# Optimization experiments

Measured on AMD Instinct MI355X. Metric: run time of the kernel, lower is better.

Reference implementation:

```python
import jax, jax.numpy as jnp
import numpy as np

N = 8192      # number of tokens/nodes
D = 256       # out_dim
E = N - 1     # one dependency triple per non-root node
ALPHA = 0.2   # LeakyReLU negative slope


def setup_inputs() -> dict:
    key = jax.random.key(0)
    k1, k2, k3, k4 = jax.random.split(key, 4)
    x = jax.random.normal(k1, (N, D), jnp.float32)
    W = jax.random.normal(k2, (D, D), jnp.float32) / np.sqrt(D)      # nn.Linear(out,out,bias=False).weight
    a = jax.random.normal(k3, (2 * D,), jnp.float32) / np.sqrt(2 * D)  # nn.Linear(2*out,1,bias=False).weight
    # each node 1..N-1 is a dependent exactly once -> h_dict keys are [0,1,...,N-1] in order
    dep = jnp.arange(1, N, dtype=jnp.int32)
    # each governor appears at most once -> each e_tensor row is softmaxed exactly once
    gov = jax.random.permutation(k4, N)[:E].astype(jnp.int32)
    return {"x": x, "W": W, "a": a, "dep": dep, "gov": gov}


def reference(x, W, a, dep, gov):
    Nn, Dd = x.shape
    neg_big = jnp.asarray(-1e18, x.dtype)
    Hx = x @ W.T  # self.weight(x[i]) for every node, [N, D]
    # per-edge attention logit: attn_weight(cat(W x_gov, W x_dep))
    s = jnp.concatenate([Hx[gov], Hx[dep]], axis=-1) @ a  # [E]
    # dense e_tensor exactly as in the module
    e = jnp.zeros((Nn, Nn), x.dtype).at[gov, dep].set(s)
    # rows belonging to a governor get masked softmax; other rows untouched
    gov_mask = jnp.zeros((Nn,), bool).at[gov].set(True)
    masked = jnp.where(e > 0, e, neg_big)
    sm = jax.nn.softmax(masked, axis=1)
    attn = jnp.where(gov_mask[:, None], sm, e)
    # self_loop/h_dict init: h[dep] = W x[gov]; node 0 stays zeros
    h = jnp.zeros((Nn, Dd), x.dtype).at[dep].set(Hx[gov])
    # aggregation: h[gov] += attn[gov, dep] * W x[dep]
    coef = attn[gov, dep]  # [E]
    h = h + jax.ops.segment_sum(coef[:, None] * Hx[dep], gov, num_segments=Nn)
    return jax.nn.leaky_relu(h, ALPHA)
```

## Files before the change

### kernel.cpp

```cpp
#include <hip/hip_runtime.h>
#include <hip/hip_bf16.h>

#define NN 8192
#define DD 256
#define EE (NN - 1)

typedef __attribute__((ext_vector_type(8))) short bf16x8;
typedef __attribute__((ext_vector_type(4))) float f32x4;

__device__ inline unsigned short f2bf(float f) {
  return __builtin_bit_cast(unsigned short, __float2bfloat16(f));
}

__global__ __launch_bounds__(1024) void prep(
    const float* __restrict__ W, const float* __restrict__ a,
    const int* __restrict__ gov,
    float* __restrict__ u, float* __restrict__ v, int* __restrict__ inv) {
  const int t = threadIdx.x;
  const int k = t & 255, part = t >> 8;

  for (int i = t; i < NN; i += 1024) inv[i] = -1;
  __syncthreads();
  for (int e = t; e < EE; e += 1024) inv[gov[e]] = e;

  float up = 0.f, vp = 0.f;
  const int j0 = part * 64;
  for (int j = j0; j < j0 + 64; ++j) {
    float w = W[(size_t)j * DD + k];
    up = fmaf(a[j], w, up);
    vp = fmaf(a[DD + j], w, vp);
  }
  __shared__ float redu[4][256], redv[4][256];
  redu[part][k] = up; redv[part][k] = vp;
  __syncthreads();
  if (t < 256) {
    u[t] = redu[0][t] + redu[1][t] + redu[2][t] + redu[3][t];
    v[t] = redv[0][t] + redv[1][t] + redv[2][t] + redv[3][t];
  }
}

__global__ __launch_bounds__(256) void pq_kernel(
    const float* __restrict__ x, const float* __restrict__ u,
    const float* __restrict__ v, float* __restrict__ p, float* __restrict__ q) {
  const int wid = threadIdx.x >> 6, lane = threadIdx.x & 63;
  const int row = blockIdx.x * 4 + wid;
  const float4 xv = *(const float4*)&x[(size_t)row * DD + lane * 4];
  const float4 uv = *(const float4*)&u[lane * 4];
  const float4 vv = *(const float4*)&v[lane * 4];
  float ps = xv.x * uv.x + xv.y * uv.y + xv.z * uv.z + xv.w * uv.w;
  float qs = xv.x * vv.x + xv.y * vv.y + xv.z * vv.z + xv.w * vv.w;
#pragma unroll
  for (int off = 32; off; off >>= 1) {
    ps += __shfl_xor(ps, off);
    qs += __shfl_xor(qs, off);
  }
  if (lane == 0) { p[row] = ps; q[row] = qs; }
}

#define BM 128
#define BN 64
#define BK 32
#define LDAB 40

__global__ __launch_bounds__(256) void gemm_mfma(
    const float* __restrict__ X, const float* __restrict__ W,
    float* __restrict__ Hx) {
  __shared__ unsigned short As[BM][LDAB];
  __shared__ unsigned short Bs[BN][LDAB];
  const int t = threadIdx.x;
  const int bm = blockIdx.x * BM, bn = blockIdx.y * BN;
  const int lane = t & 63;
  const int wid = t >> 6;
  const int wr = wid >> 1, wc = wid & 1;
  const int l15 = lane & 15, l4 = lane >> 4;

  f32x4 acc[4][2] = {};

  const int arow = t >> 1, ahalf = t & 1;
  const int brow = t >> 2, bq = t & 3;

  for (int k0 = 0; k0 < DD; k0 += BK) {
    {
      const float* src = &X[(size_t)(bm + arow) * DD + k0 + ahalf * 16];
#pragma unroll
      for (int i = 0; i < 4; ++i) {
        float4 f = *(const float4*)(src + i * 4);
        ushort4 pk;
        pk.x = f2bf(f.x); pk.y = f2bf(f.y); pk.z = f2bf(f.z); pk.w = f2bf(f.w);
        *(ushort4*)&As[arow][ahalf * 16 + i * 4] = pk;
      }
    }
    {
      const float* src = &W[(size_t)(bn + brow) * DD + k0 + bq * 8];
#pragma unroll
      for (int i = 0; i < 2; ++i) {
        float4 f = *(const float4*)(src + i * 4);
        ushort4 pk;
        pk.x = f2bf(f.x); pk.y = f2bf(f.y); pk.z = f2bf(f.z); pk.w = f2bf(f.w);
        *(ushort4*)&Bs[brow][bq * 8 + i * 4] = pk;
      }
    }
    __syncthreads();

    bf16x8 af[4], bfr[2];
#pragma unroll
    for (int mf = 0; mf < 4; ++mf)
      af[mf] = *(const bf16x8*)&As[wr * 64 + mf * 16 + l15][l4 * 8];
#pragma unroll
    for (int nf = 0; nf < 2; ++nf)
      bfr[nf] = *(const bf16x8*)&Bs[wc * 32 + nf * 16 + l15][l4 * 8];
#pragma unroll
    for (int mf = 0; mf < 4; ++mf)
#pragma unroll
      for (int nf = 0; nf < 2; ++nf)
        acc[mf][nf] = __builtin_amdgcn_mfma_f32_16x16x32_bf16(
            af[mf], bfr[nf], acc[mf][nf], 0, 0, 0);
    __syncthreads();
  }

#pragma unroll
  for (int mf = 0; mf < 4; ++mf)
#pragma unroll
    for (int nf = 0; nf < 2; ++nf)
#pragma unroll
      for (int r = 0; r < 4; ++r) {
        const int row = bm + wr * 64 + mf * 16 + l4 * 4 + r;
        const int col = bn + wc * 32 + nf * 16 + l15;
        Hx[(size_t)row * DD + col] = acc[mf][nf][r];
      }
}

__global__ __launch_bounds__(256) void finalize(
    const float* __restrict__ Hx, const float* __restrict__ p,
    const float* __restrict__ q, const int* __restrict__ gov,
    const int* __restrict__ inv, float* __restrict__ out) {
  const int sub = threadIdx.x >> 6, c4 = threadIdx.x & 63;
  const int j = blockIdx.x * 4 + sub;

  float4 h = make_float4(0.f, 0.f, 0.f, 0.f);
  if (j > 0) {
    const int g = gov[j - 1];
    h = *(const float4*)&Hx[(size_t)g * DD + c4 * 4];
  }
  const int e2 = inv[j];
  if (e2 >= 0) {
    const int d = e2 + 1;
    const float4 hd = *(const float4*)&Hx[(size_t)d * DD + c4 * 4];
    const float s = p[j] + q[d];
    const float coef = (s > 0.f) ? 1.f : (1.f / 8192.f);
    h.x = fmaf(coef, hd.x, h.x);
    h.y = fmaf(coef, hd.y, h.y);
    h.z = fmaf(coef, hd.z, h.z);
    h.w = fmaf(coef, hd.w, h.w);
  }
  float4 o;
  o.x = (h.x >= 0.f) ? h.x : 0.2f * h.x;
  o.y = (h.y >= 0.f) ? h.y : 0.2f * h.y;
  o.z = (h.z >= 0.f) ? h.z : 0.2f * h.z;
  o.w = (h.w >= 0.f) ? h.w : 0.2f * h.w;
  *(float4*)&out[(size_t)j * DD + c4 * 4] = o;
}

extern "C" void kernel_launch(void* const* d_in, const int* in_sizes, int n_in,
                              void* d_out, int out_size, void* d_ws, size_t ws_size,
                              hipStream_t stream) {
  const float* x = (const float*)d_in[0];
  const float* W = (const float*)d_in[1];
  const float* a = (const float*)d_in[2];
  const int* gov = (const int*)d_in[4];

  float* Hx = (float*)d_ws;
  float* p  = Hx + (size_t)NN * DD;
  float* q  = p + NN;
  float* u  = q + NN;
  float* v  = u + DD;
  int* inv  = (int*)(v + DD);

  hipLaunchKernelGGL(prep, dim3(1), dim3(1024), 0, stream, W, a, gov, u, v, inv);
  hipLaunchKernelGGL(pq_kernel, dim3(NN / 4), dim3(256), 0, stream, x, u, v, p, q);
  hipLaunchKernelGGL(gemm_mfma, dim3(NN / BM, DD / BN), dim3(256), 0, stream,
                     x, W, Hx);
  hipLaunchKernelGGL(finalize, dim3(NN / 4), dim3(256), 0, stream,
                     Hx, p, q, gov, inv, (float*)d_out);
}
```

Measured before the change: 101.4 us.

## Aggregate x rows before the projection GEMM and fuse LeakyReLU into its epilogue

```diff
diff --git a/kernel.cpp b/kernel.cpp
--- a/kernel.cpp
+++ b/kernel.cpp
@@ -25,6 +25,7 @@
 
   float up = 0.f, vp = 0.f;
   const int j0 = part * 64;
+#pragma unroll 4
   for (int j = j0; j < j0 + 64; ++j) {
     float w = W[(size_t)j * DD + k];
     up = fmaf(a[j], w, up);
@@ -57,60 +58,81 @@
   if (lane == 0) { p[row] = ps; q[row] = qs; }
 }
 
-#define BM 128
+__global__ __launch_bounds__(256) void combine(
+    const float* __restrict__ x, const float* __restrict__ p,
+    const float* __restrict__ q, const int* __restrict__ gov,
+    const int* __restrict__ inv, unsigned short* __restrict__ y) {
+  const int sub = threadIdx.x >> 6, lane = threadIdx.x & 63;
+  const int j = blockIdx.x * 4 + sub;
+
+  float4 h = make_float4(0.f, 0.f, 0.f, 0.f);
+  if (j > 0) {
+    const int g = gov[j - 1];
+    h = *(const float4*)&x[(size_t)g * DD + lane * 4];
+  }
+  const int e2 = inv[j];
+  if (e2 >= 0) {
+    const int d = e2 + 1;
+    const float4 xd = *(const float4*)&x[(size_t)d * DD + lane * 4];
+    const float s = p[j] + q[d];
+    const float coef = (s > 0.f) ? 1.f : (1.f / 8192.f);
+    h.x = fmaf(coef, xd.x, h.x);
+    h.y = fmaf(coef, xd.y, h.y);
+    h.z = fmaf(coef, xd.z, h.z);
+    h.w = fmaf(coef, xd.w, h.w);
+  }
+  ushort4 pk;
+  pk.x = f2bf(h.x); pk.y = f2bf(h.y); pk.z = f2bf(h.z); pk.w = f2bf(h.w);
+  *(ushort4*)&y[(size_t)j * DD + lane * 4] = pk;
+}
+
+#define BM 64
 #define BN 64
 #define BK 32
 #define LDAB 40
 
-__global__ __launch_bounds__(256) void gemm_mfma(
-    const float* __restrict__ X, const float* __restrict__ W,
-    float* __restrict__ Hx) {
+__global__ __launch_bounds__(256) void gemm_out(
+    const unsigned short* __restrict__ Y, const float* __restrict__ W,
+    float* __restrict__ out) {
   __shared__ unsigned short As[BM][LDAB];
   __shared__ unsigned short Bs[BN][LDAB];
   const int t = threadIdx.x;
   const int bm = blockIdx.x * BM, bn = blockIdx.y * BN;
-  const int lane = t & 63;
-  const int wid = t >> 6;
+  const int lane = t & 63, wid = t >> 6;
   const int wr = wid >> 1, wc = wid & 1;
   const int l15 = lane & 15, l4 = lane >> 4;
+  const int srow = t >> 2, sseg = t & 3;
 
-  f32x4 acc[4][2] = {};
-
-  const int arow = t >> 1, ahalf = t & 1;
-  const int brow = t >> 2, bq = t & 3;
+  f32x4 acc[2][2] = {};
 
   for (int k0 = 0; k0 < DD; k0 += BK) {
     {
-      const float* src = &X[(size_t)(bm + arow) * DD + k0 + ahalf * 16];
-#pragma unroll
-      for (int i = 0; i < 4; ++i) {
-        float4 f = *(const float4*)(src + i * 4);
-        ushort4 pk;
-        pk.x = f2bf(f.x); pk.y = f2bf(f.y); pk.z = f2bf(f.z); pk.w = f2bf(f.w);
-        *(ushort4*)&As[arow][ahalf * 16 + i * 4] = pk;
-      }
+      ushort4 w0 = *(const ushort4*)&Y[(size_t)(bm + srow) * DD + k0 + sseg * 8];
+      ushort4 w1 = *(const ushort4*)&Y[(size_t)(bm + srow) * DD + k0 + sseg * 8 + 4];
+      *(ushort4*)&As[srow][sseg * 8] = w0;
+      *(ushort4*)&As[srow][sseg * 8 + 4] = w1;
     }
     {
-      const float* src = &W[(size_t)(bn + brow) * DD + k0 + bq * 8];
-#pragma unroll
-      for (int i = 0; i < 2; ++i) {
-        float4 f = *(const float4*)(src + i * 4);
-        ushort4 pk;
-        pk.x = f2bf(f.x); pk.y = f2bf(f.y); pk.z = f2bf(f.z); pk.w = f2bf(f.w);
-        *(ushort4*)&Bs[brow][bq * 8 + i * 4] = pk;
-      }
+      const float* src = &W[(size_t)(bn + srow) * DD + k0 + sseg * 8];
+      float4 f0 = *(const float4*)src;
+      float4 f1 = *(const float4*)(src + 4);
+      ushort4 p0, p1;
+      p0.x = f2bf(f0.x); p0.y = f2bf(f0.y); p0.z = f2bf(f0.z); p0.w = f2bf(f0.w);
+      p1.x = f2bf(f1.x); p1.y = f2bf(f1.y); p1.z = f2bf(f1.z); p1.w = f2bf(f1.w);
+      *(ushort4*)&Bs[srow][sseg * 8] = p0;
+      *(ushort4*)&Bs[srow][sseg * 8 + 4] = p1;
     }
     __syncthreads();
 
-    bf16x8 af[4], bfr[2];
+    bf16x8 af[2], bfr[2];
 #pragma unroll
-    for (int mf = 0; mf < 4; ++mf)
-      af[mf] = *(const bf16x8*)&As[wr * 64 + mf * 16 + l15][l4 * 8];
+    for (int mf = 0; mf < 2; ++mf)
+      af[mf] = *(const bf16x8*)&As[wr * 32 + mf * 16 + l15][l4 * 8];
 #pragma unroll
     for (int nf = 0; nf < 2; ++nf)
       bfr[nf] = *(const bf16x8*)&Bs[wc * 32 + nf * 16 + l15][l4 * 8];
 #pragma unroll
-    for (int mf = 0; mf < 4; ++mf)
+    for (int mf = 0; mf < 2; ++mf)
 #pragma unroll
       for (int nf = 0; nf < 2; ++nf)
         acc[mf][nf] = __builtin_amdgcn_mfma_f32_16x16x32_bf16(
@@ -119,46 +141,16 @@
   }
 
 #pragma unroll
-  for (int mf = 0; mf < 4; ++mf)
+  for (int mf = 0; mf < 2; ++mf)
 #pragma unroll
     for (int nf = 0; nf < 2; ++nf)
 #pragma unroll
       for (int r = 0; r < 4; ++r) {
-        const int row = bm + wr * 64 + mf * 16 + l4 * 4 + r;
+        const int row = bm + wr * 32 + mf * 16 + l4 * 4 + r;
         const int col = bn + wc * 32 + nf * 16 + l15;
-        Hx[(size_t)row * DD + col] = acc[mf][nf][r];
+        float hval = acc[mf][nf][r];
+        out[(size_t)row * DD + col] = (hval >= 0.f) ? hval : 0.2f * hval;
       }
-}
-
-__global__ __launch_bounds__(256) void finalize(
-    const float* __restrict__ Hx, const float* __restrict__ p,
-    const float* __restrict__ q, const int* __restrict__ gov,
-    const int* __restrict__ inv, float* __restrict__ out) {
-  const int sub = threadIdx.x >> 6, c4 = threadIdx.x & 63;
-  const int j = blockIdx.x * 4 + sub;
-
-  float4 h = make_float4(0.f, 0.f, 0.f, 0.f);
-  if (j > 0) {
-    const int g = gov[j - 1];
-    h = *(const float4*)&Hx[(size_t)g * DD + c4 * 4];
-  }
-  const int e2 = inv[j];
-  if (e2 >= 0) {
-    const int d = e2 + 1;
-    const float4 hd = *(const float4*)&Hx[(size_t)d * DD + c4 * 4];
-    const float s = p[j] + q[d];
-    const float coef = (s > 0.f) ? 1.f : (1.f / 8192.f);
-    h.x = fmaf(coef, hd.x, h.x);
-    h.y = fmaf(coef, hd.y, h.y);
-    h.z = fmaf(coef, hd.z, h.z);
-    h.w = fmaf(coef, hd.w, h.w);
-  }
-  float4 o;
-  o.x = (h.x >= 0.f) ? h.x : 0.2f * h.x;
-  o.y = (h.y >= 0.f) ? h.y : 0.2f * h.y;
-  o.z = (h.z >= 0.f) ? h.z : 0.2f * h.z;
-  o.w = (h.w >= 0.f) ? h.w : 0.2f * h.w;
-  *(float4*)&out[(size_t)j * DD + c4 * 4] = o;
 }
 
 extern "C" void kernel_launch(void* const* d_in, const int* in_sizes, int n_in,
@@ -169,17 +161,17 @@
   const float* a = (const float*)d_in[2];
   const int* gov = (const int*)d_in[4];
 
-  float* Hx = (float*)d_ws;
-  float* p  = Hx + (size_t)NN * DD;
-  float* q  = p + NN;
-  float* u  = q + NN;
-  float* v  = u + DD;
-  int* inv  = (int*)(v + DD);
+  float* p = (float*)d_ws;
+  float* q = p + NN;
+  float* u = q + NN;
+  float* v = u + DD;
+  int* inv = (int*)(v + DD);
+  unsigned short* y = (unsigned short*)(inv + NN);
 
   hipLaunchKernelGGL(prep, dim3(1), dim3(1024), 0, stream, W, a, gov, u, v, inv);
   hipLaunchKernelGGL(pq_kernel, dim3(NN / 4), dim3(256), 0, stream, x, u, v, p, q);
-  hipLaunchKernelGGL(gemm_mfma, dim3(NN / BM, DD / BN), dim3(256), 0, stream,
-                     x, W, Hx);
-  hipLaunchKernelGGL(finalize, dim3(NN / 4), dim3(256), 0, stream,
-                     Hx, p, q, gov, inv, (float*)d_out);
+  hipLaunchKernelGGL(combine, dim3(NN / 4), dim3(256), 0, stream,
+                     x, p, q, gov, inv, y);
+  hipLaunchKernelGGL(gemm_out, dim3(NN / BM, DD / BN), dim3(256), 0, stream,
+                     y, W, (float*)d_out);
 }
```

Result: faster. 96.94 us (-4.4%).
